# Performance work log

Hardware: AMD Instinct MI355X
Metric: run time of the kernel (lower is better)

## Reference

```python
import jax, jax.numpy as jnp
import numpy as np
from jax import lax

B, T, C = 256, 128, 512
HID, HOR = 1024, 96
THR = 1.0


def setup_inputs() -> dict:
    key = jax.random.key(0)
    ks = jax.random.split(key, 6)
    x = jax.random.normal(ks[0], (B, T, C), dtype=jnp.float32)
    # fc1: Linear(C -> HID), PyTorch layout [out, in]
    W1 = jax.random.normal(ks[1], (HID, C), dtype=jnp.float32) / np.sqrt(C)
    b1 = jax.random.normal(ks[2], (HID,), dtype=jnp.float32) * 0.01
    # head: Linear(HID -> HOR)
    Wh = jax.random.normal(ks[3], (HOR, HID), dtype=jnp.float32) / np.sqrt(HID)
    bh = jax.random.normal(ks[4], (HOR,), dtype=jnp.float32) * 0.01
    beta = jnp.float32(0.9)  # learnable leak (snntorch Leaky, learn_beta=True)
    return {"x": x, "W1": W1, "b1": b1, "Wh": Wh, "bh": bh, "beta": beta}


def reference(x, W1, b1, Wh, bh, beta):
    # Precompute all fc1 projections as one batched GEMM: [B,T,HID]
    proj = jnp.einsum("btc,hc->bth", x, W1) + b1
    beta_c = jnp.clip(beta, 0.0, 1.0)

    def step(mem, inp):
        # snntorch Leaky, reset_mechanism='subtract': reset based on PREVIOUS mem
        reset = (mem > THR).astype(mem.dtype)  # detached in snntorch
        mem_new = beta_c * mem + inp - reset * THR
        return mem_new, None

    mem0 = jnp.zeros((x.shape[0], W1.shape[0]), dtype=x.dtype)
    mem_T, _ = lax.scan(step, mem0, jnp.moveaxis(proj, 1, 0))  # scan over T
    return mem_T @ Wh.T + bh  # [B, HOR]
```

## Files before the change

kernel.cpp:

```cpp
#include <hip/hip_runtime.h>

#define TT 128
#define CC 512
#define HIDN 1024
#define HORN 96
#define NB 256
#define BN 128
#define BK 64
#define NSTAGE 8

typedef _Float16 f16x8 __attribute__((ext_vector_type(8)));
typedef _Float16 f16x4 __attribute__((ext_vector_type(4)));
typedef float f32x16 __attribute__((ext_vector_type(16)));

#define XHI 0
#define XLO 16384
#define WHI 32768
#define WLO 49152
#define SMEM_BYTES 65536

__device__ __forceinline__ void cvt_split(const float4 v, f16x4* hi, f16x4* lo) {
    auto h01 = __builtin_amdgcn_cvt_pkrtz(v.x, v.y);
    auto h23 = __builtin_amdgcn_cvt_pkrtz(v.z, v.w);
    auto l01 = __builtin_amdgcn_cvt_pkrtz(v.x - (float)h01.x, v.y - (float)h01.y);
    auto l23 = __builtin_amdgcn_cvt_pkrtz(v.z - (float)h23.x, v.w - (float)h23.y);
    *hi = (f16x4){(_Float16)h01.x, (_Float16)h01.y, (_Float16)h23.x, (_Float16)h23.y};
    *lo = (f16x4){(_Float16)l01.x, (_Float16)l01.y, (_Float16)l23.x, (_Float16)l23.y};
}

__device__ __forceinline__ void gload16(const void* g, void* l) {
    __builtin_amdgcn_global_load_lds(
        (const __attribute__((address_space(1))) unsigned int*)g,
        (__attribute__((address_space(3))) unsigned int*)l, 16, 0, 0);
}

__global__ void __launch_bounds__(256)
snn_cvtw(const float* __restrict__ W1, f16x4* __restrict__ whi, f16x4* __restrict__ wlo,
         const float* __restrict__ bh, float* __restrict__ out)
{
    const int i = blockIdx.x * 256 + threadIdx.x;
    const float4 v = ((const float4*)W1)[i];
    f16x4 hi, lo;
    cvt_split(v, &hi, &lo);
    whi[i] = hi;
    wlo[i] = lo;
    if (i < NB * HORN) out[i] = bh[i % HORN];
}

__global__ void __launch_bounds__(256, 2)
snn_proj_scan(const float* __restrict__ x, const _Float16* __restrict__ whi_g,
              const _Float16* __restrict__ wlo_g, const float* __restrict__ b1,
              const float* __restrict__ betap, float* __restrict__ memT)
{
    __shared__ __align__(16) char smem[SMEM_BYTES];

    const int tid  = threadIdx.x;
    const int lane = tid & 63;
    const int wid  = tid >> 6;
    const int wm = wid >> 1, wn = wid & 1;
    const int g2 = lane >> 5, lr = lane & 31;

    const int lid  = blockIdx.x;
    const int slot = lid >> 3;
    const int b     = ((lid & 7) << 5) + (slot >> 3);
    const int hbase = (slot & 7) * BN;

    const float* __restrict__ xg = x + (size_t)b * TT * CC;

    const int srow = tid >> 4;
    const int skq  = tid & 15;
    const float* xrow = xg + srow * CC + skq * 4;
    const int wbyte = (skq * 8) ^ ((srow & 7) << 4);

    const int wrow0  = lane >> 3;
    const int wslotb = ((lane & 7) ^ wrow0) * 16;
    const char* whsrc = (const char*)whi_g + ((size_t)(hbase + wrow0) * CC) * 2 + wslotb;
    const char* wlsrc = (const char*)wlo_g + ((size_t)(hbase + wrow0) * CC) * 2 + wslotb;

    const int sw    = (lr & 7) << 4;
    const int arow0 = (wm * 64 +  0 + lr) * 128;
    const int arow1 = (wm * 64 + 32 + lr) * 128;
    const int brow0 = (wn * 64 +  0 + lr) * 128;
    const int brow1 = (wn * 64 + 32 + lr) * 128;

    f32x16 acc00 = {}, acc01 = {}, acc10 = {}, acc11 = {};

    float4 px[8];
#pragma unroll
    for (int p = 0; p < 8; ++p) px[p] = *(const float4*)(xrow + p * 16 * CC);

#define FRAG_SET(P) f16x8 ah0##P, ah1##P, al0##P, al1##P, bh0##P, bh1##P, bl0##P, bl1##P;
#define FRAG_LOAD(P, KS) { \
        const int off = (((KS) << 5) | (g2 << 4)) ^ sw; \
        ah0##P = *(const f16x8*)(smem + XHI + arow0 + off); \
        ah1##P = *(const f16x8*)(smem + XHI + arow1 + off); \
        al0##P = *(const f16x8*)(smem + XLO + arow0 + off); \
        al1##P = *(const f16x8*)(smem + XLO + arow1 + off); \
        bh0##P = *(const f16x8*)(smem + WHI + brow0 + off); \
        bh1##P = *(const f16x8*)(smem + WHI + brow1 + off); \
        bl0##P = *(const f16x8*)(smem + WLO + brow0 + off); \
        bl1##P = *(const f16x8*)(smem + WLO + brow1 + off); }
#define FRAG_MFMA(P) \
        acc00 = __builtin_amdgcn_mfma_f32_32x32x16_f16(ah0##P, bh0##P, acc00, 0, 0, 0); \
        acc01 = __builtin_amdgcn_mfma_f32_32x32x16_f16(ah0##P, bh1##P, acc01, 0, 0, 0); \
        acc10 = __builtin_amdgcn_mfma_f32_32x32x16_f16(ah1##P, bh0##P, acc10, 0, 0, 0); \
        acc11 = __builtin_amdgcn_mfma_f32_32x32x16_f16(ah1##P, bh1##P, acc11, 0, 0, 0); \
        acc00 = __builtin_amdgcn_mfma_f32_32x32x16_f16(ah0##P, bl0##P, acc00, 0, 0, 0); \
        acc01 = __builtin_amdgcn_mfma_f32_32x32x16_f16(ah0##P, bl1##P, acc01, 0, 0, 0); \
        acc10 = __builtin_amdgcn_mfma_f32_32x32x16_f16(ah1##P, bl0##P, acc10, 0, 0, 0); \
        acc11 = __builtin_amdgcn_mfma_f32_32x32x16_f16(ah1##P, bl1##P, acc11, 0, 0, 0); \
        acc00 = __builtin_amdgcn_mfma_f32_32x32x16_f16(al0##P, bh0##P, acc00, 0, 0, 0); \
        acc01 = __builtin_amdgcn_mfma_f32_32x32x16_f16(al0##P, bh1##P, acc01, 0, 0, 0); \
        acc10 = __builtin_amdgcn_mfma_f32_32x32x16_f16(al1##P, bh0##P, acc10, 0, 0, 0); \
        acc11 = __builtin_amdgcn_mfma_f32_32x32x16_f16(al1##P, bh1##P, acc11, 0, 0, 0);

    for (int s = 0; s < NSTAGE; ++s) {
#pragma unroll
        for (int c = 0; c < 4; ++c) {
            const int chunk = wid * 4 + c;
            const size_t go = (size_t)chunk * (8 * CC * 2) + (size_t)s * (BK * 2);
            gload16(whsrc + go, smem + WHI + chunk * 1024);
            gload16(wlsrc + go, smem + WLO + chunk * 1024);
        }
#pragma unroll
        for (int p = 0; p < 8; ++p) {
            const int byte = (srow + 16 * p) * 128 + wbyte;
            f16x4 hi, lo;
            cvt_split(px[p], &hi, &lo);
            *(f16x4*)(smem + XHI + byte) = hi;
            *(f16x4*)(smem + XLO + byte) = lo;
        }
        __syncthreads();

        if (s + 1 < NSTAGE) {
            const int ko = (s + 1) * BK;
#pragma unroll
            for (int p = 0; p < 8; ++p)
                px[p] = *(const float4*)(xrow + p * 16 * CC + ko);
        }

        {
            FRAG_SET(A)
            FRAG_SET(B)
            FRAG_LOAD(A, 0)
            FRAG_LOAD(B, 1)
            __builtin_amdgcn_s_setprio(1);
            FRAG_MFMA(A)
            FRAG_LOAD(A, 2)
            FRAG_MFMA(B)
            FRAG_LOAD(B, 3)
            FRAG_MFMA(A)
            FRAG_MFMA(B)
            __builtin_amdgcn_s_setprio(0);
        }
        __syncthreads();
    }
#undef FRAG_SET
#undef FRAG_LOAD
#undef FRAG_MFMA

#define ST_ACC(A, m, n) {                                                        \
        const int row   = wn * 64 + (n) * 32 + lr;                               \
        const int sbase = wm * 16 + (m) * 8 + g2;                                \
        const int rs    = row & 31;                                              \
        char* rb = smem + row * 512;                                             \
        *(float4*)(rb + (((sbase + 0) ^ rs) * 16)) = make_float4(A[0],  A[1],  A[2],  A[3]);  \
        *(float4*)(rb + (((sbase + 2) ^ rs) * 16)) = make_float4(A[4],  A[5],  A[6],  A[7]);  \
        *(float4*)(rb + (((sbase + 4) ^ rs) * 16)) = make_float4(A[8],  A[9],  A[10], A[11]); \
        *(float4*)(rb + (((sbase + 6) ^ rs) * 16)) = make_float4(A[12], A[13], A[14], A[15]); }
    ST_ACC(acc00, 0, 0)
    ST_ACC(acc01, 0, 1)
    ST_ACC(acc10, 1, 0)
    ST_ACC(acc11, 1, 1)
#undef ST_ACC
    __syncthreads();

    if (tid < BN) {
        const float beta_c = fminf(fmaxf(betap[0], 0.0f), 1.0f);
        const float b1h = b1[hbase + tid];
        const char* rb = smem + tid * 512;
        const int rs = tid & 31;
        float mem = 0.0f;
#pragma unroll
        for (int q = 0; q < 32; ++q) {
            const float4 v = *(const float4*)(rb + ((q ^ rs) * 16));
            float reset;
            reset = (mem > 1.0f) ? 1.0f : 0.0f; mem = beta_c * mem + (v.x + b1h) - reset;
            reset = (mem > 1.0f) ? 1.0f : 0.0f; mem = beta_c * mem + (v.y + b1h) - reset;
            reset = (mem > 1.0f) ? 1.0f : 0.0f; mem = beta_c * mem + (v.z + b1h) - reset;
            reset = (mem > 1.0f) ? 1.0f : 0.0f; mem = beta_c * mem + (v.w + b1h) - reset;
        }
        memT[(size_t)b * HIDN + hbase + tid] = mem;
    }
}

__global__ void __launch_bounds__(256)
snn_head(const float* __restrict__ memT, const float* __restrict__ Wh,
         float* __restrict__ out)
{
    __shared__ __align__(16) float ms[16][64];
    __shared__ __align__(16) float ws[HORN][64];
    const int tid = threadIdx.x;
    const int kc = blockIdx.x, bg = blockIdx.y;
    const int kof = kc * 64;

    {
        const int row = tid >> 4, c4 = tid & 15;
        *(float4*)&ms[row][c4 * 4] =
            *(const float4*)(memT + (size_t)(bg * 16 + row) * HIDN + kof + c4 * 4);
    }
#pragma unroll
    for (int r = 0; r < 6; ++r) {
        const int q = r * 256 + tid;
        const int row = q >> 4, c4 = q & 15;
        *(float4*)&ws[row][c4 * 4] =
            *(const float4*)(Wh + (size_t)row * HIDN + kof + c4 * 4);
    }
    __syncthreads();

#pragma unroll
    for (int r = 0; r < 6; ++r) {
        const int p = r * 256 + tid;
        const int bb = p / HORN, o = p % HORN;
        const float4* mv = (const float4*)&ms[bb][0];
        const float4* wv = (const float4*)&ws[o][0];
        float a = 0.0f;
#pragma unroll
        for (int q = 0; q < 16; ++q) {
            const float4 w = wv[q];
            const float4 m = mv[q];
            a = fmaf(w.x, m.x, fmaf(w.y, m.y, fmaf(w.z, m.z, fmaf(w.w, m.w, a))));
        }
        atomicAdd(out + (size_t)(bg * 16 + bb) * HORN + o, a);
    }
}

extern "C" void kernel_launch(void* const* d_in, const int* in_sizes, int n_in,
                              void* d_out, int out_size, void* d_ws, size_t ws_size,
                              hipStream_t stream)
{
    (void)in_sizes; (void)n_in; (void)out_size; (void)ws_size;
    const float* x    = (const float*)d_in[0];
    const float* W1   = (const float*)d_in[1];
    const float* b1   = (const float*)d_in[2];
    const float* Wh   = (const float*)d_in[3];
    const float* bh   = (const float*)d_in[4];
    const float* beta = (const float*)d_in[5];

    char* ws = (char*)d_ws;
    _Float16* whi = (_Float16*)(ws);
    _Float16* wlo = (_Float16*)(ws + (1 << 20));
    float*    memT = (float*)(ws + (2 << 20));
    float*    out  = (float*)d_out;

    snn_cvtw<<<512, 256, 0, stream>>>(W1, (f16x4*)whi, (f16x4*)wlo, bh, out);
    snn_proj_scan<<<2048, 256, 0, stream>>>(x, whi, wlo, b1, beta, memT);
    snn_head<<<dim3(16, 16), 256, 0, stream>>>(memT, Wh, out);
}
```

Before: 212.4 us.

## Double-buffer async LDS loads, widen tile to 256 HID, split x in-register

The projection-scan kernel now uses 512-thread blocks covering 256 hidden units per batch row, with BK=32 over 16 stages. Shared memory is double-buffered and x and W tiles are both fetched with direct global-to-LDS loads one stage ahead. The fp32 x tiles are stored raw in LDS and split into hi/lo fp16 at fragment-load time instead of before the store. The scan epilogue runs in two halves over the wider tile. This aims to overlap global loads with MFMA work and halve redundant x traffic, at the cost of more LDS per block, one block per CU, and repeated hi/lo conversion in every warp.

```diff
diff --git a/kernel.cpp b/kernel.cpp
--- a/kernel.cpp
+++ b/kernel.cpp
@@ -5,19 +5,18 @@
 #define HIDN 1024
 #define HORN 96
 #define NB 256
-#define BN 128
-#define BK 64
-#define NSTAGE 8
+#define BM 128
+#define BN 256
+#define BK 32
+#define NSTAGE 16
 
 typedef _Float16 f16x8 __attribute__((ext_vector_type(8)));
 typedef _Float16 f16x4 __attribute__((ext_vector_type(4)));
 typedef float f32x16 __attribute__((ext_vector_type(16)));
 
-#define XHI 0
-#define XLO 16384
-#define WHI 32768
-#define WLO 49152
-#define SMEM_BYTES 65536
+#define BUFSZ 49152
+#define WOFF  16384
+#define SMEM_BYTES 98304
 
 __device__ __forceinline__ void cvt_split(const float4 v, f16x4* hi, f16x4* lo) {
     auto h01 = __builtin_amdgcn_cvt_pkrtz(v.x, v.y);
@@ -28,6 +27,22 @@
     *lo = (f16x4){(_Float16)l01.x, (_Float16)l01.y, (_Float16)l23.x, (_Float16)l23.y};
 }
 
+__device__ __forceinline__ void cvt_split8(const float4 f0, const float4 f1,
+                                           f16x8* hi, f16x8* lo) {
+    auto h0 = __builtin_amdgcn_cvt_pkrtz(f0.x, f0.y);
+    auto h1 = __builtin_amdgcn_cvt_pkrtz(f0.z, f0.w);
+    auto h2 = __builtin_amdgcn_cvt_pkrtz(f1.x, f1.y);
+    auto h3 = __builtin_amdgcn_cvt_pkrtz(f1.z, f1.w);
+    auto l0 = __builtin_amdgcn_cvt_pkrtz(f0.x - (float)h0.x, f0.y - (float)h0.y);
+    auto l1 = __builtin_amdgcn_cvt_pkrtz(f0.z - (float)h1.x, f0.w - (float)h1.y);
+    auto l2 = __builtin_amdgcn_cvt_pkrtz(f1.x - (float)h2.x, f1.y - (float)h2.y);
+    auto l3 = __builtin_amdgcn_cvt_pkrtz(f1.z - (float)h3.x, f1.w - (float)h3.y);
+    *hi = (f16x8){(_Float16)h0.x, (_Float16)h0.y, (_Float16)h1.x, (_Float16)h1.y,
+                  (_Float16)h2.x, (_Float16)h2.y, (_Float16)h3.x, (_Float16)h3.y};
+    *lo = (f16x8){(_Float16)l0.x, (_Float16)l0.y, (_Float16)l1.x, (_Float16)l1.y,
+                  (_Float16)l2.x, (_Float16)l2.y, (_Float16)l3.x, (_Float16)l3.y};
+}
+
 __device__ __forceinline__ void gload16(const void* g, void* l) {
     __builtin_amdgcn_global_load_lds(
         (const __attribute__((address_space(1))) unsigned int*)g,
@@ -47,7 +62,7 @@
     if (i < NB * HORN) out[i] = bh[i % HORN];
 }
 
-__global__ void __launch_bounds__(256, 2)
+__global__ void __launch_bounds__(512, 1)
 snn_proj_scan(const float* __restrict__ x, const _Float16* __restrict__ whi_g,
               const _Float16* __restrict__ wlo_g, const float* __restrict__ b1,
               const float* __restrict__ betap, float* __restrict__ memT)
@@ -57,141 +72,130 @@
     const int tid  = threadIdx.x;
     const int lane = tid & 63;
     const int wid  = tid >> 6;
-    const int wm = wid >> 1, wn = wid & 1;
+    const int wm = wid >> 2, wn = wid & 3;
     const int g2 = lane >> 5, lr = lane & 31;
-
-    const int lid  = blockIdx.x;
-    const int slot = lid >> 3;
-    const int b     = ((lid & 7) << 5) + (slot >> 3);
-    const int hbase = (slot & 7) * BN;
-
-    const float* __restrict__ xg = x + (size_t)b * TT * CC;
-
-    const int srow = tid >> 4;
-    const int skq  = tid & 15;
-    const float* xrow = xg + srow * CC + skq * 4;
-    const int wbyte = (skq * 8) ^ ((srow & 7) << 4);
-
-    const int wrow0  = lane >> 3;
-    const int wslotb = ((lane & 7) ^ wrow0) * 16;
-    const char* whsrc = (const char*)whi_g + ((size_t)(hbase + wrow0) * CC) * 2 + wslotb;
-    const char* wlsrc = (const char*)wlo_g + ((size_t)(hbase + wrow0) * CC) * 2 + wslotb;
-
-    const int sw    = (lr & 7) << 4;
-    const int arow0 = (wm * 64 +  0 + lr) * 128;
-    const int arow1 = (wm * 64 + 32 + lr) * 128;
-    const int brow0 = (wn * 64 +  0 + lr) * 128;
-    const int brow1 = (wn * 64 + 32 + lr) * 128;
+    const int am = lr & 7;
+
+    const int lid = blockIdx.x;
+    const int idx = lid >> 3;
+    const int b     = ((lid & 7) << 5) + (idx >> 2);
+    const int hbase = (idx & 3) * BN;
+
+    const int rr = lane >> 3, pp = lane & 7;
+    const int uu = pp ^ rr;
+    const char* xgc = (const char*)(x + (size_t)b * TT * CC);
+    const char* xsrc0 = xgc + (size_t)(16 * wid + rr) * 2048 + uu * 16;
+    const char* xsrc1 = xgc + (size_t)(16 * wid + 8 + rr) * 2048 + uu * 16;
+    const char* wbase = (uu < 4) ? (const char*)whi_g : (const char*)wlo_g;
+    const char* wsrc0 = wbase + (size_t)(hbase + 32 * wid + rr) * 1024 + (uu & 3) * 16;
+    const char* wsrc1 = wsrc0 + 8 * 1024;
+    const char* wsrc2 = wsrc0 + 16 * 1024;
+    const char* wsrc3 = wsrc0 + 24 * 1024;
+
+    const int arow0 = (wm * 64 + lr) * 128;
+    const int arow1 = arow0 + 32 * 128;
+    const int brow0 = WOFF + (wn * 64 + lr) * 128;
+    const int brow1 = brow0 + 32 * 128;
 
     f32x16 acc00 = {}, acc01 = {}, acc10 = {}, acc11 = {};
 
-    float4 px[8];
-#pragma unroll
-    for (int p = 0; p < 8; ++p) px[p] = *(const float4*)(xrow + p * 16 * CC);
-
-#define FRAG_SET(P) f16x8 ah0##P, ah1##P, al0##P, al1##P, bh0##P, bh1##P, bl0##P, bl1##P;
-#define FRAG_LOAD(P, KS) { \
-        const int off = (((KS) << 5) | (g2 << 4)) ^ sw; \
-        ah0##P = *(const f16x8*)(smem + XHI + arow0 + off); \
-        ah1##P = *(const f16x8*)(smem + XHI + arow1 + off); \
-        al0##P = *(const f16x8*)(smem + XLO + arow0 + off); \
-        al1##P = *(const f16x8*)(smem + XLO + arow1 + off); \
-        bh0##P = *(const f16x8*)(smem + WHI + brow0 + off); \
-        bh1##P = *(const f16x8*)(smem + WHI + brow1 + off); \
-        bl0##P = *(const f16x8*)(smem + WLO + brow0 + off); \
-        bl1##P = *(const f16x8*)(smem + WLO + brow1 + off); }
-#define FRAG_MFMA(P) \
-        acc00 = __builtin_amdgcn_mfma_f32_32x32x16_f16(ah0##P, bh0##P, acc00, 0, 0, 0); \
-        acc01 = __builtin_amdgcn_mfma_f32_32x32x16_f16(ah0##P, bh1##P, acc01, 0, 0, 0); \
-        acc10 = __builtin_amdgcn_mfma_f32_32x32x16_f16(ah1##P, bh0##P, acc10, 0, 0, 0); \
-        acc11 = __builtin_amdgcn_mfma_f32_32x32x16_f16(ah1##P, bh1##P, acc11, 0, 0, 0); \
-        acc00 = __builtin_amdgcn_mfma_f32_32x32x16_f16(ah0##P, bl0##P, acc00, 0, 0, 0); \
-        acc01 = __builtin_amdgcn_mfma_f32_32x32x16_f16(ah0##P, bl1##P, acc01, 0, 0, 0); \
-        acc10 = __builtin_amdgcn_mfma_f32_32x32x16_f16(ah1##P, bl0##P, acc10, 0, 0, 0); \
-        acc11 = __builtin_amdgcn_mfma_f32_32x32x16_f16(ah1##P, bl1##P, acc11, 0, 0, 0); \
-        acc00 = __builtin_amdgcn_mfma_f32_32x32x16_f16(al0##P, bh0##P, acc00, 0, 0, 0); \
-        acc01 = __builtin_amdgcn_mfma_f32_32x32x16_f16(al0##P, bh1##P, acc01, 0, 0, 0); \
-        acc10 = __builtin_amdgcn_mfma_f32_32x32x16_f16(al1##P, bh0##P, acc10, 0, 0, 0); \
-        acc11 = __builtin_amdgcn_mfma_f32_32x32x16_f16(al1##P, bh1##P, acc11, 0, 0, 0);
-
+#define STAGE_LOADS(S, BB) { \
+        gload16(xsrc0 + (S) * 128, smem + (BB) + (2 * wid) * 1024); \
+        gload16(xsrc1 + (S) * 128, smem + (BB) + (2 * wid + 1) * 1024); \
+        gload16(wsrc0 + (S) * 64,  smem + (BB) + WOFF + (4 * wid) * 1024); \
+        gload16(wsrc1 + (S) * 64,  smem + (BB) + WOFF + (4 * wid + 1) * 1024); \
+        gload16(wsrc2 + (S) * 64,  smem + (BB) + WOFF + (4 * wid + 2) * 1024); \
+        gload16(wsrc3 + (S) * 64,  smem + (BB) + WOFF + (4 * wid + 3) * 1024); }
+
+#define KSTEP(CUR, KS) { \
+        const int ua16 = (((KS) * 4 + g2 * 2) ^ am) << 4; \
+        const int ub16 = (((KS) * 2 + g2) ^ am) << 4; \
+        const float4 a00 = *(const float4*)(smem + (CUR) + arow0 + ua16); \
+        const float4 a01 = *(const float4*)(smem + (CUR) + arow0 + (ua16 ^ 16)); \
+        const float4 a10 = *(const float4*)(smem + (CUR) + arow1 + ua16); \
+        const float4 a11 = *(const float4*)(smem + (CUR) + arow1 + (ua16 ^ 16)); \
+        const f16x8 bh0 = *(const f16x8*)(smem + (CUR) + brow0 + ub16); \
+        const f16x8 bl0 = *(const f16x8*)(smem + (CUR) + brow0 + (ub16 ^ 64)); \
+        const f16x8 bh1 = *(const f16x8*)(smem + (CUR) + brow1 + ub16); \
+        const f16x8 bl1 = *(const f16x8*)(smem + (CUR) + brow1 + (ub16 ^ 64)); \
+        f16x8 ah0, al0, ah1, al1; \
+        cvt_split8(a00, a01, &ah0, &al0); \
+        cvt_split8(a10, a11, &ah1, &al1); \
+        acc00 = __builtin_amdgcn_mfma_f32_32x32x16_f16(ah0, bh0, acc00, 0, 0, 0); \
+        acc01 = __builtin_amdgcn_mfma_f32_32x32x16_f16(ah0, bh1, acc01, 0, 0, 0); \
+        acc10 = __builtin_amdgcn_mfma_f32_32x32x16_f16(ah1, bh0, acc10, 0, 0, 0); \
+        acc11 = __builtin_amdgcn_mfma_f32_32x32x16_f16(ah1, bh1, acc11, 0, 0, 0); \
+        acc00 = __builtin_amdgcn_mfma_f32_32x32x16_f16(ah0, bl0, acc00, 0, 0, 0); \
+        acc01 = __builtin_amdgcn_mfma_f32_32x32x16_f16(ah0, bl1, acc01, 0, 0, 0); \
+        acc10 = __builtin_amdgcn_mfma_f32_32x32x16_f16(ah1, bl0, acc10, 0, 0, 0); \
+        acc11 = __builtin_amdgcn_mfma_f32_32x32x16_f16(ah1, bl1, acc11, 0, 0, 0); \
+        acc00 = __builtin_amdgcn_mfma_f32_32x32x16_f16(al0, bh0, acc00, 0, 0, 0); \
+        acc01 = __builtin_amdgcn_mfma_f32_32x32x16_f16(al0, bh1, acc01, 0, 0, 0); \
+        acc10 = __builtin_amdgcn_mfma_f32_32x32x16_f16(al1, bh0, acc10, 0, 0, 0); \
+        acc11 = __builtin_amdgcn_mfma_f32_32x32x16_f16(al1, bh1, acc11, 0, 0, 0); }
+
+    STAGE_LOADS(0, 0)
+    asm volatile("s_waitcnt vmcnt(0)" ::: "memory");
+    __builtin_amdgcn_s_barrier();
+
+#pragma unroll
     for (int s = 0; s < NSTAGE; ++s) {
-#pragma unroll
-        for (int c = 0; c < 4; ++c) {
-            const int chunk = wid * 4 + c;
-            const size_t go = (size_t)chunk * (8 * CC * 2) + (size_t)s * (BK * 2);
-            gload16(whsrc + go, smem + WHI + chunk * 1024);
-            gload16(wlsrc + go, smem + WLO + chunk * 1024);
-        }
-#pragma unroll
-        for (int p = 0; p < 8; ++p) {
-            const int byte = (srow + 16 * p) * 128 + wbyte;
-            f16x4 hi, lo;
-            cvt_split(px[p], &hi, &lo);
-            *(f16x4*)(smem + XHI + byte) = hi;
-            *(f16x4*)(smem + XLO + byte) = lo;
+        const int cur = (s & 1) ? BUFSZ : 0;
+        const int nxt = (s & 1) ? 0 : BUFSZ;
+        if (s + 1 < NSTAGE) STAGE_LOADS(s + 1, nxt)
+        __builtin_amdgcn_sched_barrier(0);
+        __builtin_amdgcn_s_setprio(1);
+        KSTEP(cur, 0)
+        KSTEP(cur, 1)
+        __builtin_amdgcn_s_setprio(0);
+        asm volatile("s_waitcnt vmcnt(0)" ::: "memory");
+        __builtin_amdgcn_s_barrier();
+    }
+#undef KSTEP
+#undef STAGE_LOADS
+
+#define ST_ACC(A, a, bb, wl) { \
+        const int row = (wl) * 64 + (bb) * 32 + lr; \
+        const int sb  = wm * 16 + (a) * 8 + g2; \
+        const int rs  = row & 31; \
+        char* rb = smem + row * 512; \
+        *(float4*)(rb + (((sb + 0) ^ rs) * 16)) = make_float4(A[0],  A[1],  A[2],  A[3]);  \
+        *(float4*)(rb + (((sb + 2) ^ rs) * 16)) = make_float4(A[4],  A[5],  A[6],  A[7]);  \
+        *(float4*)(rb + (((sb + 4) ^ rs) * 16)) = make_float4(A[8],  A[9],  A[10], A[11]); \
+        *(float4*)(rb + (((sb + 6) ^ rs) * 16)) = make_float4(A[12], A[13], A[14], A[15]); }
+
+    const float beta_c = fminf(fmaxf(betap[0], 0.0f), 1.0f);
+
+#pragma unroll
+    for (int half = 0; half < 2; ++half) {
+        if ((wn >> 1) == half) {
+            const int wl = wn & 1;
+            ST_ACC(acc00, 0, 0, wl)
+            ST_ACC(acc01, 0, 1, wl)
+            ST_ACC(acc10, 1, 0, wl)
+            ST_ACC(acc11, 1, 1, wl)
         }
         __syncthreads();
-
-        if (s + 1 < NSTAGE) {
-            const int ko = (s + 1) * BK;
-#pragma unroll
-            for (int p = 0; p < 8; ++p)
-                px[p] = *(const float4*)(xrow + p * 16 * CC + ko);
-        }
-
-        {
-            FRAG_SET(A)
-            FRAG_SET(B)
-            FRAG_LOAD(A, 0)
-            FRAG_LOAD(B, 1)
-            __builtin_amdgcn_s_setprio(1);
-            FRAG_MFMA(A)
-            FRAG_LOAD(A, 2)
-            FRAG_MFMA(B)
-            FRAG_LOAD(B, 3)
-            FRAG_MFMA(A)
-            FRAG_MFMA(B)
-            __builtin_amdgcn_s_setprio(0);
+        if (tid < 128) {
+            const int hg = hbase + half * 128 + tid;
+            const float b1h = b1[hg];
+            const char* rb = smem + tid * 512;
+            const int rs = tid & 31;
+            float mem = 0.0f;
+#pragma unroll
+            for (int q = 0; q < 32; ++q) {
+                const float4 v = *(const float4*)(rb + ((q ^ rs) * 16));
+                float reset;
+                reset = (mem > 1.0f) ? 1.0f : 0.0f; mem = beta_c * mem + (v.x + b1h) - reset;
+                reset = (mem > 1.0f) ? 1.0f : 0.0f; mem = beta_c * mem + (v.y + b1h) - reset;
+                reset = (mem > 1.0f) ? 1.0f : 0.0f; mem = beta_c * mem + (v.z + b1h) - reset;
+                reset = (mem > 1.0f) ? 1.0f : 0.0f; mem = beta_c * mem + (v.w + b1h) - reset;
+            }
+            memT[(size_t)b * HIDN + hg] = mem;
         }
         __syncthreads();
     }
-#undef FRAG_SET
-#undef FRAG_LOAD
-#undef FRAG_MFMA
-
-#define ST_ACC(A, m, n) {                                                        \
-        const int row   = wn * 64 + (n) * 32 + lr;                               \
-        const int sbase = wm * 16 + (m) * 8 + g2;                                \
-        const int rs    = row & 31;                                              \
-        char* rb = smem + row * 512;                                             \
-        *(float4*)(rb + (((sbase + 0) ^ rs) * 16)) = make_float4(A[0],  A[1],  A[2],  A[3]);  \
-        *(float4*)(rb + (((sbase + 2) ^ rs) * 16)) = make_float4(A[4],  A[5],  A[6],  A[7]);  \
-        *(float4*)(rb + (((sbase + 4) ^ rs) * 16)) = make_float4(A[8],  A[9],  A[10], A[11]); \
-        *(float4*)(rb + (((sbase + 6) ^ rs) * 16)) = make_float4(A[12], A[13], A[14], A[15]); }
-    ST_ACC(acc00, 0, 0)
-    ST_ACC(acc01, 0, 1)
-    ST_ACC(acc10, 1, 0)
-    ST_ACC(acc11, 1, 1)
 #undef ST_ACC
-    __syncthreads();
-
-    if (tid < BN) {
-        const float beta_c = fminf(fmaxf(betap[0], 0.0f), 1.0f);
-        const float b1h = b1[hbase + tid];
-        const char* rb = smem + tid * 512;
-        const int rs = tid & 31;
-        float mem = 0.0f;
-#pragma unroll
-        for (int q = 0; q < 32; ++q) {
-            const float4 v = *(const float4*)(rb + ((q ^ rs) * 16));
-            float reset;
-            reset = (mem > 1.0f) ? 1.0f : 0.0f; mem = beta_c * mem + (v.x + b1h) - reset;
-            reset = (mem > 1.0f) ? 1.0f : 0.0f; mem = beta_c * mem + (v.y + b1h) - reset;
-            reset = (mem > 1.0f) ? 1.0f : 0.0f; mem = beta_c * mem + (v.z + b1h) - reset;
-            reset = (mem > 1.0f) ? 1.0f : 0.0f; mem = beta_c * mem + (v.w + b1h) - reset;
-        }
-        memT[(size_t)b * HIDN + hbase + tid] = mem;
-    }
 }
 
 __global__ void __launch_bounds__(256)
@@ -248,12 +252,12 @@
     const float* beta = (const float*)d_in[5];
 
     char* ws = (char*)d_ws;
-    _Float16* whi = (_Float16*)(ws);
-    _Float16* wlo = (_Float16*)(ws + (1 << 20));
+    _Float16* whi  = (_Float16*)(ws);
+    _Float16* wlo  = (_Float16*)(ws + (1 << 20));
     float*    memT = (float*)(ws + (2 << 20));
     float*    out  = (float*)d_out;
 
     snn_cvtw<<<512, 256, 0, stream>>>(W1, (f16x4*)whi, (f16x4*)wlo, bh, out);
-    snn_proj_scan<<<2048, 256, 0, stream>>>(x, whi, wlo, b1, beta, memT);
+    snn_proj_scan<<<1024, 512, 0, stream>>>(x, whi, wlo, b1, beta, memT);
     snn_head<<<dim3(16, 16), 256, 0, stream>>>(memT, Wh, out);
 }
```

Measured after the change: 232.4 us. +9.4%, slower.
